# Kernel tuning notes

Measured on AMD Instinct MI355X. Metric: run time of the kernel, lower is better.

Reference implementation:

```python
import jax, jax.numpy as jnp
import numpy as np

N_NODES = 100000


def setup_inputs() -> dict:
    key = jax.random.key(0)
    k1, k2, k3 = jax.random.split(key, 3)
    feat = jax.random.normal(k1, (N_NODES, 64), dtype=jnp.float32)
    src = jax.random.randint(k2, (1250000,), 0, N_NODES, dtype=jnp.int64)
    dst = jax.random.randint(k3, (1250000,), 0, N_NODES, dtype=jnp.int64)
    return {"feat": feat, "src": src, "dst": dst}


def reference(feat, src, dst):
    # GraphConv(norm='both', activation=None): degree-normalized neighbor sum
    # with implicit self-connection (rst = feat_dst + sum_neighbors), where
    # degrees are clamp(min=1) + 1 to account for the self edge.
    n = feat.shape[0]
    ones = jnp.ones(src.shape[0], dtype=feat.dtype)
    out_deg = jax.ops.segment_sum(ones, src, num_segments=n)
    in_deg = jax.ops.segment_sum(ones, dst, num_segments=n)
    norm_l = jax.lax.rsqrt(jnp.maximum(out_deg, 1.0) + 1.0)  # [N]
    norm_r = jax.lax.rsqrt(jnp.maximum(in_deg, 1.0) + 1.0)   # [N]
    feat_src = feat * norm_l[:, None]                         # left-normalize
    msgs = feat_src[src]                                      # gather [E, D]
    h_neigh = jax.ops.segment_sum(msgs, dst, num_segments=n)  # scatter-sum [N, D]
    rst = (feat + h_neigh) * norm_r[:, None]                  # right-normalize
    return rst
```

## Files before the change

kernel.cpp:

```cpp
#include <hip/hip_runtime.h>


#define GC_D 64
#define PSIZE 196
#define SCAP 3072
#define EPB 8192
#define MAXPART 512
#define GC_CAP 64


__global__ __launch_bounds__(512) void partition_kernel(
        const int* __restrict__ src,
        const int* __restrict__ dst,
        int* __restrict__ curA,
        int* __restrict__ curB,
        int* __restrict__ streamA,
        unsigned char* __restrict__ streamB,
        int e, int nPart) {
    __shared__ int histA[MAXPART], histB[MAXPART], baseA[MAXPART], baseB[MAXPART];
    __shared__ int lcurA[MAXPART], lcurB[MAXPART];
    int t = threadIdx.x;
    for (int i = t; i < nPart; i += 512) {
        histA[i] = 0; histB[i] = 0; lcurA[i] = 0; lcurB[i] = 0;
    }
    __syncthreads();
    int lo = blockIdx.x * EPB;
    int hi = min(lo + EPB, e);
    for (int i = lo + t; i < hi; i += 512) {
        int s = src[i], d = dst[i];
        atomicAdd(&histA[d / PSIZE], 1);
        atomicAdd(&histB[s / PSIZE], 1);
    }
    __syncthreads();
    for (int i = t; i < nPart; i += 512) {
        int hA = histA[i];
        baseA[i] = hA ? atomicAdd(&curA[i], hA) : 0;
        int hB = histB[i];
        baseB[i] = hB ? atomicAdd(&curB[i], hB) : 0;
    }
    __syncthreads();
    for (int i = lo + t; i < hi; i += 512) {
        int s = src[i], d = dst[i];
        int pA = d / PSIZE;
        int posA = baseA[pA] + atomicAdd(&lcurA[pA], 1);
        if (posA < SCAP) streamA[pA * SCAP + posA] = s | ((d - pA * PSIZE) << 17);
        int pB = s / PSIZE;
        int posB = baseB[pB] + atomicAdd(&lcurB[pB], 1);
        if (posB < SCAP) streamB[pB * SCAP + posB] = (unsigned char)(s - pB * PSIZE);
    }
}

__global__ __launch_bounds__(512) void convertB_kernel(
        const int* __restrict__ curB,
        const unsigned char* __restrict__ streamB,
        const float* __restrict__ feat,
        unsigned short* __restrict__ featb,
        int n) {
    __shared__ int lodeg[256];
    int p = blockIdx.x, t = threadIdx.x;
    if (t < 256) lodeg[t] = 0;
    __syncthreads();
    int cB = min(curB[p], SCAP);
    const unsigned char* sB = streamB + (size_t)p * SCAP;
    for (int i = t; i < cB; i += 512) atomicAdd(&lodeg[sB[i]], 1);
    __syncthreads();
    int wave = t >> 6, lane = t & 63;
    int g = p * PSIZE;
    for (int r = wave; r < PSIZE; r += 8) {
        int node = g + r;
        if (node >= n) break;
        float nl = rsqrtf(fmaxf((float)lodeg[r], 1.0f) + 1.0f);
        float v = feat[(size_t)node * GC_D + lane] * nl;
        unsigned bb = __float_as_uint(v);
        bb = (bb + 0x7FFFu + ((bb >> 16) & 1u)) >> 16;
        featb[(size_t)node * GC_D + lane] = (unsigned short)bb;
    }
    if (p == 0 && t < GC_D) featb[(size_t)n * GC_D + t] = 0;
}

__global__ __launch_bounds__(1024) void sortgather_kernel(
        const int* __restrict__ curA,
        const int* __restrict__ streamA,
        const float* __restrict__ feat,
        const unsigned short* __restrict__ featb,
        float* __restrict__ out,
        int n) {
    __shared__ int sAl[SCAP];
    __shared__ int lperm[SCAP];
    __shared__ int lcnt[256], loff[256], lcur[256];
    int p = blockIdx.x, t = threadIdx.x;
    if (t < 256) lcnt[t] = 0;
    __syncthreads();
    int cA = min(curA[p], SCAP);
    const int* sA = streamA + (size_t)p * SCAP;
    for (int i = t; i < cA; i += 1024) {
        int v = sA[i];
        sAl[i] = v;
        atomicAdd(&lcnt[(v >> 17) & 255], 1);
    }
    __syncthreads();
    if (t < 256) loff[t] = lcnt[t];
    __syncthreads();
    for (int off = 1; off < 256; off <<= 1) {
        int a = (t < 256 && t >= off) ? loff[t - off] : 0;
        __syncthreads();
        if (t < 256) loff[t] += a;
        __syncthreads();
    }
    if (t < 256) { loff[t] -= lcnt[t]; lcur[t] = 0; }
    __syncthreads();
    for (int i = t; i < cA; i += 1024) {
        int v = sAl[i];
        int bin = (v >> 17) & 255;
        int pos = loff[bin] + atomicAdd(&lcur[bin], 1);
        lperm[pos] = v & 0x1FFFF;
    }
    __syncthreads();
    int wave = t >> 6, lane = t & 63;
    int half = lane >> 5;
    int c = lane & 31;
    int g = p * PSIZE;
    for (int r = wave; r < PSIZE; r += 16) {
        int node = g + r;
        if (node >= n) break;
        int deg = lcnt[r];
        int off = loff[r];
        float acc0 = 0.0f, acc1 = 0.0f;
        for (int base = 0; base < deg; base += 64) {
            int m = min(deg - base, 64);
            int s_l = (lane < m) ? lperm[off + base + lane] : n;
            int m16 = (m + 15) & ~15;
            for (int j = 0; j < m16; j += 16) {
#pragma unroll
                for (int k = 0; k < 8; ++k) {
                    int s = __shfl(s_l, j + 2 * k + half);
                    unsigned u = *(const unsigned*)(featb + (size_t)s * GC_D + 2 * c);
                    acc0 += __uint_as_float(u << 16);
                    acc1 += __uint_as_float(u & 0xFFFF0000u);
                }
            }
        }
        acc0 += __shfl_xor(acc0, 32);
        acc1 += __shfl_xor(acc1, 32);
        if (half == 0) {
            float nr = rsqrtf(fmaxf((float)deg, 1.0f) + 1.0f);
            const float2 self = *(const float2*)(feat + (size_t)node * GC_D + 2 * c);
            float2 rr;
            rr.x = (self.x + acc0) * nr;
            rr.y = (self.y + acc1) * nr;
            *(float2*)(out + (size_t)node * GC_D + 2 * c) = rr;
        }
    }
}


__global__ void zero_int_kernel(int* __restrict__ p, int n) {
    int i = blockIdx.x * blockDim.x + threadIdx.x;
    if (i < n) p[i] = 0;
}

__global__ void bucket_hist_kernel(const int* __restrict__ src,
                                   const int* __restrict__ dst,
                                   int* __restrict__ cnt,
                                   int* __restrict__ outdeg,
                                   int* __restrict__ bucket,
                                   int e) {
    int i = blockIdx.x * blockDim.x + threadIdx.x;
    if (i < e) {
        int s = src[i];
        int d = dst[i];
        atomicAdd(&outdeg[s], 1);
        int pos = atomicAdd(&cnt[d], 1);
        if (pos < GC_CAP) bucket[d * GC_CAP + pos] = s;
    }
}

__global__ void convert_kernel(const float* __restrict__ feat,
                               const int* __restrict__ outdeg,
                               unsigned short* __restrict__ featb,
                               int n) {
    int i = blockIdx.x * blockDim.x + threadIdx.x;
    int total = (n + 1) * GC_D;
    if (i >= total) return;
    int row = i >> 6;
    if (row >= n) { featb[i] = 0; return; }
    float nl = rsqrtf(fmaxf((float)outdeg[row], 1.0f) + 1.0f);
    unsigned b = __float_as_uint(feat[i] * nl);
    b = (b + 0x7FFFu + ((b >> 16) & 1u)) >> 16;
    featb[i] = (unsigned short)b;
}

__global__ __launch_bounds__(256) void gather_bf16_kernel(
        const float* __restrict__ feat,
        const unsigned short* __restrict__ featb,
        const int* __restrict__ bucket,
        const int* __restrict__ cnt,
        float* __restrict__ out,
        int n) {
    int wid = (blockIdx.x * blockDim.x + threadIdx.x) >> 6;
    int lane = threadIdx.x & 63;
    if (wid >= n) return;
    int deg = cnt[wid];
    int s_raw = bucket[wid * GC_CAP + lane];
    int m = min(deg, GC_CAP);
    int s_l = (lane < m) ? s_raw : n;
    int half = lane >> 5;
    int c = lane & 31;
    float acc0 = 0.0f, acc1 = 0.0f;
    int m16 = (m + 15) & ~15;
    for (int j = 0; j < m16; j += 16) {
#pragma unroll
        for (int k = 0; k < 8; ++k) {
            int s = __shfl(s_l, j + 2 * k + half);
            unsigned u = *(const unsigned*)(featb + (size_t)s * GC_D + 2 * c);
            acc0 += __uint_as_float(u << 16);
            acc1 += __uint_as_float(u & 0xFFFF0000u);
        }
    }
    acc0 += __shfl_xor(acc0, 32);
    acc1 += __shfl_xor(acc1, 32);
    if (half == 0) {
        float nr = rsqrtf(fmaxf((float)deg, 1.0f) + 1.0f);
        const float2 self = *(const float2*)(feat + (size_t)wid * GC_D + 2 * c);
        float2 r;
        r.x = (self.x + acc0) * nr;
        r.y = (self.y + acc1) * nr;
        *(float2*)(out + (size_t)wid * GC_D + 2 * c) = r;
    }
}


extern "C" void kernel_launch(void* const* d_in, const int* in_sizes, int n_in,
                              void* d_out, int out_size, void* d_ws, size_t ws_size,
                              hipStream_t stream) {
    const float* feat = (const float*)d_in[0];
    const int*   src  = (const int*)d_in[1];
    const int*   dst  = (const int*)d_in[2];
    float* out = (float*)d_out;

    const int n = in_sizes[0] / GC_D;
    const int e = in_sizes[1];
    const int nPart = (n + PSIZE - 1) / PSIZE;

    size_t featb_ints = ((size_t)(n + 1) * GC_D + 1) / 2;
    size_t o = 2 * (size_t)nPart;
    o = (o + 31) & ~(size_t)31;
    size_t streamA_o = o;  o += (size_t)nPart * SCAP;
    size_t featb_o = o;    o += featb_ints;
    size_t need_main = o * sizeof(int) + (size_t)nPart * SCAP;

    size_t featb_bytes = (size_t)(n + 1) * GC_D * sizeof(unsigned short);
    size_t need_bf16 = ((size_t)2 * n + (size_t)n * GC_CAP) * sizeof(int) + featb_bytes;

    bool main_ok = (ws_size >= need_main) && nPart <= MAXPART && n <= 131071;

    if (main_ok) {
        int* ws = (int*)d_ws;
        int* curA = ws;
        int* curB = ws + nPart;
        int* streamA = ws + streamA_o;
        unsigned short* featb = (unsigned short*)(ws + featb_o);
        unsigned char* streamB = (unsigned char*)(ws + o);

        hipMemsetAsync(curA, 0, 2 * (size_t)nPart * sizeof(int), stream);
        partition_kernel<<<(e + EPB - 1) / EPB, 512, 0, stream>>>(
            src, dst, curA, curB, streamA, streamB, e, nPart);
        convertB_kernel<<<nPart, 512, 0, stream>>>(curB, streamB, feat, featb, n);
        sortgather_kernel<<<nPart, 1024, 0, stream>>>(curA, streamA, feat, featb,
                                                      out, n);
    } else if (ws_size >= need_bf16) {
        int* cnt    = (int*)d_ws;
        int* outdeg = cnt + n;
        int* bucket = outdeg + n;
        unsigned short* featb = (unsigned short*)(bucket + (size_t)n * GC_CAP);

        zero_int_kernel<<<(2 * n + 255) / 256, 256, 0, stream>>>(cnt, 2 * n);
        bucket_hist_kernel<<<(e + 255) / 256, 256, 0, stream>>>(src, dst, cnt,
                                                                outdeg, bucket, e);
        int totalc = (n + 1) * GC_D;
        convert_kernel<<<(totalc + 255) / 256, 256, 0, stream>>>(feat, outdeg,
                                                                 featb, n);
        long long total = (long long)n * GC_D;
        gather_bf16_kernel<<<(int)((total + 255) / 256), 256, 0, stream>>>(
            feat, featb, bucket, cnt, out, n);
    }
}
```

Measured before the change: 156.3 us.

## Compute out-degree with global atomics, drop source-partition stream, vectorize convert

Replaces the second partitioned byte stream (streamB) and its per-partition shared-memory histogram kernel with direct global atomicAdd on a per-node outdeg array during partitioning. The convert step becomes a flat, float4-vectorized kernel that reads outdeg, and partition blocks shrink (EPB lowered) so more blocks run. This removes a scatter write stream and one shared-memory pass, but the global atomics are random and may contend, and the smaller blocks add more global curA atomics.

```diff
diff --git a/kernel.cpp b/kernel.cpp
--- a/kernel.cpp
+++ b/kernel.cpp
@@ -4,7 +4,7 @@
 #define GC_D 64
 #define PSIZE 196
 #define SCAP 3072
-#define EPB 8192
+#define EPB 2442
 #define MAXPART 512
 #define GC_CAP 64
 
@@ -13,30 +13,24 @@
         const int* __restrict__ src,
         const int* __restrict__ dst,
         int* __restrict__ curA,
-        int* __restrict__ curB,
+        int* __restrict__ outdeg,
         int* __restrict__ streamA,
-        unsigned char* __restrict__ streamB,
         int e, int nPart) {
-    __shared__ int histA[MAXPART], histB[MAXPART], baseA[MAXPART], baseB[MAXPART];
-    __shared__ int lcurA[MAXPART], lcurB[MAXPART];
+    __shared__ int histA[MAXPART], baseA[MAXPART], lcurA[MAXPART];
     int t = threadIdx.x;
-    for (int i = t; i < nPart; i += 512) {
-        histA[i] = 0; histB[i] = 0; lcurA[i] = 0; lcurB[i] = 0;
-    }
+    for (int i = t; i < nPart; i += 512) { histA[i] = 0; lcurA[i] = 0; }
     __syncthreads();
     int lo = blockIdx.x * EPB;
     int hi = min(lo + EPB, e);
     for (int i = lo + t; i < hi; i += 512) {
         int s = src[i], d = dst[i];
         atomicAdd(&histA[d / PSIZE], 1);
-        atomicAdd(&histB[s / PSIZE], 1);
+        atomicAdd(&outdeg[s], 1);
     }
     __syncthreads();
     for (int i = t; i < nPart; i += 512) {
         int hA = histA[i];
         baseA[i] = hA ? atomicAdd(&curA[i], hA) : 0;
-        int hB = histB[i];
-        baseB[i] = hB ? atomicAdd(&curB[i], hB) : 0;
     }
     __syncthreads();
     for (int i = lo + t; i < hi; i += 512) {
@@ -44,38 +38,36 @@
         int pA = d / PSIZE;
         int posA = baseA[pA] + atomicAdd(&lcurA[pA], 1);
         if (posA < SCAP) streamA[pA * SCAP + posA] = s | ((d - pA * PSIZE) << 17);
-        int pB = s / PSIZE;
-        int posB = baseB[pB] + atomicAdd(&lcurB[pB], 1);
-        if (posB < SCAP) streamB[pB * SCAP + posB] = (unsigned char)(s - pB * PSIZE);
-    }
-}
-
-__global__ __launch_bounds__(512) void convertB_kernel(
-        const int* __restrict__ curB,
-        const unsigned char* __restrict__ streamB,
+    }
+}
+
+__device__ __forceinline__ unsigned short to_bf16_rne(float v) {
+    unsigned b = __float_as_uint(v);
+    b = (b + 0x7FFFu + ((b >> 16) & 1u)) >> 16;
+    return (unsigned short)b;
+}
+
+__global__ __launch_bounds__(256) void convert_kernel(
         const float* __restrict__ feat,
+        const int* __restrict__ outdeg,
         unsigned short* __restrict__ featb,
         int n) {
-    __shared__ int lodeg[256];
-    int p = blockIdx.x, t = threadIdx.x;
-    if (t < 256) lodeg[t] = 0;
-    __syncthreads();
-    int cB = min(curB[p], SCAP);
-    const unsigned char* sB = streamB + (size_t)p * SCAP;
-    for (int i = t; i < cB; i += 512) atomicAdd(&lodeg[sB[i]], 1);
-    __syncthreads();
-    int wave = t >> 6, lane = t & 63;
-    int g = p * PSIZE;
-    for (int r = wave; r < PSIZE; r += 8) {
-        int node = g + r;
-        if (node >= n) break;
-        float nl = rsqrtf(fmaxf((float)lodeg[r], 1.0f) + 1.0f);
-        float v = feat[(size_t)node * GC_D + lane] * nl;
-        unsigned bb = __float_as_uint(v);
-        bb = (bb + 0x7FFFu + ((bb >> 16) & 1u)) >> 16;
-        featb[(size_t)node * GC_D + lane] = (unsigned short)bb;
-    }
-    if (p == 0 && t < GC_D) featb[(size_t)n * GC_D + t] = 0;
+    int i = blockIdx.x * 256 + threadIdx.x;
+    int row = i >> 4;
+    if (row > n) return;
+    if (row == n) {
+        ushort4 z; z.x = 0; z.y = 0; z.z = 0; z.w = 0;
+        *(ushort4*)(featb + (size_t)i * 4) = z;
+        return;
+    }
+    float nl = rsqrtf(fmaxf((float)outdeg[row], 1.0f) + 1.0f);
+    float4 v = *(const float4*)(feat + (size_t)i * 4);
+    ushort4 r;
+    r.x = to_bf16_rne(v.x * nl);
+    r.y = to_bf16_rne(v.y * nl);
+    r.z = to_bf16_rne(v.z * nl);
+    r.w = to_bf16_rne(v.w * nl);
+    *(ushort4*)(featb + (size_t)i * 4) = r;
 }
 
 __global__ __launch_bounds__(1024) void sortgather_kernel(
@@ -175,21 +167,6 @@
     }
 }
 
-__global__ void convert_kernel(const float* __restrict__ feat,
-                               const int* __restrict__ outdeg,
-                               unsigned short* __restrict__ featb,
-                               int n) {
-    int i = blockIdx.x * blockDim.x + threadIdx.x;
-    int total = (n + 1) * GC_D;
-    if (i >= total) return;
-    int row = i >> 6;
-    if (row >= n) { featb[i] = 0; return; }
-    float nl = rsqrtf(fmaxf((float)outdeg[row], 1.0f) + 1.0f);
-    unsigned b = __float_as_uint(feat[i] * nl);
-    b = (b + 0x7FFFu + ((b >> 16) & 1u)) >> 16;
-    featb[i] = (unsigned short)b;
-}
-
 __global__ __launch_bounds__(256) void gather_bf16_kernel(
         const float* __restrict__ feat,
         const unsigned short* __restrict__ featb,
@@ -243,11 +220,11 @@
     const int nPart = (n + PSIZE - 1) / PSIZE;
 
     size_t featb_ints = ((size_t)(n + 1) * GC_D + 1) / 2;
-    size_t o = 2 * (size_t)nPart;
+    size_t o = (size_t)nPart + (size_t)n;
     o = (o + 31) & ~(size_t)31;
     size_t streamA_o = o;  o += (size_t)nPart * SCAP;
     size_t featb_o = o;    o += featb_ints;
-    size_t need_main = o * sizeof(int) + (size_t)nPart * SCAP;
+    size_t need_main = o * sizeof(int);
 
     size_t featb_bytes = (size_t)(n + 1) * GC_D * sizeof(unsigned short);
     size_t need_bf16 = ((size_t)2 * n + (size_t)n * GC_CAP) * sizeof(int) + featb_bytes;
@@ -257,15 +234,16 @@
     if (main_ok) {
         int* ws = (int*)d_ws;
         int* curA = ws;
-        int* curB = ws + nPart;
+        int* outdeg = ws + nPart;
         int* streamA = ws + streamA_o;
         unsigned short* featb = (unsigned short*)(ws + featb_o);
-        unsigned char* streamB = (unsigned char*)(ws + o);
-
-        hipMemsetAsync(curA, 0, 2 * (size_t)nPart * sizeof(int), stream);
+
+        hipMemsetAsync(curA, 0, ((size_t)nPart + n) * sizeof(int), stream);
         partition_kernel<<<(e + EPB - 1) / EPB, 512, 0, stream>>>(
-            src, dst, curA, curB, streamA, streamB, e, nPart);
-        convertB_kernel<<<nPart, 512, 0, stream>>>(curB, streamB, feat, featb, n);
+            src, dst, curA, outdeg, streamA, e, nPart);
+        int conv_threads = (n + 1) * 16;
+        convert_kernel<<<(conv_threads + 255) / 256, 256, 0, stream>>>(
+            feat, outdeg, featb, n);
         sortgather_kernel<<<nPart, 1024, 0, stream>>>(curA, streamA, feat, featb,
                                                       out, n);
     } else if (ws_size >= need_bf16) {
@@ -277,9 +255,9 @@
         zero_int_kernel<<<(2 * n + 255) / 256, 256, 0, stream>>>(cnt, 2 * n);
         bucket_hist_kernel<<<(e + 255) / 256, 256, 0, stream>>>(src, dst, cnt,
                                                                 outdeg, bucket, e);
-        int totalc = (n + 1) * GC_D;
-        convert_kernel<<<(totalc + 255) / 256, 256, 0, stream>>>(feat, outdeg,
-                                                                 featb, n);
+        int conv_threads = (n + 1) * 16;
+        convert_kernel<<<(conv_threads + 255) / 256, 256, 0, stream>>>(
+            feat, outdeg, featb, n);
         long long total = (long long)n * GC_D;
         gather_bf16_kernel<<<(int)((total + 255) / 256), 256, 0, stream>>>(
             feat, featb, bucket, cnt, out, n);
```

After: 183.3 us. 17.2% more time.
